# Kernel tuning notes

Measured on AMD Instinct MI355X. Metric: run time of the kernel, lower is better.

## Reference

```python
import jax, jax.numpy as jnp
import numpy as np

SEED_ID = 1234  # seed_id from init, masked to 32 bits


def _synth_R(k_iter, d_out, d_in, dtype):
    # Seeded pseudo-random base weight: randn(d_out, d_in) / sqrt(d_in)
    s = (SEED_ID ^ int(k_iter)) & 0xFFFFFFFF
    R = jax.random.normal(jax.random.key(s), (d_out, d_in), dtype=dtype)
    return R * np.float32(1.0 / np.sqrt(d_in))


def setup_inputs() -> dict:
    key = jax.random.key(0)
    kx, kv, ku = jax.random.split(key, 3)
    B, S, D, RANK = 32, 4096, 512, 64
    x = jax.random.normal(kx, (B, S, D), dtype=jnp.float32)
    alpha = jnp.float32(1.0)
    U = jnp.zeros((D, RANK), dtype=jnp.float32)
    # match torch init: V ~ N(0,1)/sqrt(rank)
    V = jax.random.normal(kv, (RANK, D), dtype=jnp.float32) * np.float32(1.0 / np.sqrt(RANK))
    bias = jnp.zeros((D,), dtype=jnp.float32)
    return {"x": x, "alpha": alpha, "U": U, "V": V, "bias": bias, "k_iter": 2}


def reference(x, alpha, U, V, bias, k_iter):
    d_out = U.shape[0]
    d_in = V.shape[1]
    dtype = x.dtype
    R = _synth_R(k_iter, d_out, d_in, dtype)                      # [d_out, d_in]
    W = alpha.astype(dtype) * R + (U.astype(dtype) @ V.astype(dtype))  # [d_out, d_in]
    # F.linear: x @ W.T + b
    return jnp.einsum('bsd,od->bso', x, W) + bias.astype(dtype)
```

## Files before the change

kernel.cpp:

```cpp
#include <hip/hip_runtime.h>
#include <stdint.h>


#define M_TOTAL 131072
#define N_DIM 512
#define K_DIM 512
#define RANK 64

#define BM 128
#define BK 32
#define NKT (K_DIM / BK)

#define AOFF(p) ((p)*16384)
#define WOFF(p) (32768 + (p)*32768)

typedef __attribute__((ext_vector_type(8))) short bf16x8;
typedef __attribute__((ext_vector_type(4))) float f32x4;

__device__ __forceinline__ void threefry2x32(uint32_t k0, uint32_t k1,
                                             uint32_t x0, uint32_t x1,
                                             uint32_t& y0, uint32_t& y1) {
  uint32_t ks2 = k0 ^ k1 ^ 0x1BD11BDAu;
  const uint32_t ks[3] = {k0, k1, ks2};
  const int R0[4] = {13, 15, 26, 6};
  const int R1[4] = {17, 29, 16, 24};
  x0 += ks[0];
  x1 += ks[1];
#pragma unroll
  for (int g = 0; g < 5; ++g) {
    const int* r = (g & 1) ? R1 : R0;
#pragma unroll
    for (int i = 0; i < 4; ++i) {
      x0 += x1;
      x1 = (x1 << r[i]) | (x1 >> (32 - r[i]));
      x1 ^= x0;
    }
    x0 += ks[(g + 1) % 3];
    x1 += ks[(g + 2) % 3] + (uint32_t)(g + 1);
  }
  y0 = x0;
  y1 = x1;
}

__device__ __forceinline__ float erfinv_f32(float x) {
  float w = -log1pf(-x * x);
  float p;
  if (w < 5.0f) {
    w = w - 2.5f;
    p = 2.81022636e-08f;
    p = fmaf(p, w, 3.43273939e-07f);
    p = fmaf(p, w, -3.5233877e-06f);
    p = fmaf(p, w, -4.39150654e-06f);
    p = fmaf(p, w, 0.00021858087f);
    p = fmaf(p, w, -0.00125372503f);
    p = fmaf(p, w, -0.00417768164f);
    p = fmaf(p, w, 0.246640727f);
    p = fmaf(p, w, 1.50140941f);
  } else {
    w = sqrtf(w) - 3.0f;
    p = -0.000200214257f;
    p = fmaf(p, w, 0.000100950558f);
    p = fmaf(p, w, 0.00134934322f);
    p = fmaf(p, w, -0.00367342844f);
    p = fmaf(p, w, 0.00573950773f);
    p = fmaf(p, w, -0.0076224613f);
    p = fmaf(p, w, 0.00943887047f);
    p = fmaf(p, w, 1.00167406f);
    p = fmaf(p, w, 2.83297682f);
  }
  return p * x;
}

__device__ __forceinline__ unsigned short f32_to_bf16_rtne(float f) {
  uint32_t x = __float_as_uint(f);
  uint32_t r = (x + 0x7FFFu + ((x >> 16) & 1u)) >> 16;
  return (unsigned short)r;
}

__global__ __launch_bounds__(256) void build_w_kernel(
    const float* __restrict__ alpha_p, const float* __restrict__ U,
    const float* __restrict__ V, const int* __restrict__ k_iter_p,
    unsigned short* __restrict__ Wb) {
  int idx = blockIdx.x * blockDim.x + threadIdx.x;
  uint32_t s = (1234u ^ (uint32_t)(*k_iter_p));
  uint32_t y0, y1;
  threefry2x32(0u, s, 0u, (uint32_t)idx, y0, y1);
  uint32_t bits = y0 ^ y1;
  float u01 = __uint_as_float((bits >> 9) | 0x3f800000u) - 1.0f;
  const float lo = -0.99999994f;
  float u = fmaxf(lo, u01 * 2.0f + lo);
  float rnorm = 1.41421354f * erfinv_f32(u);
  const float scale = 0.044194173824159216f;

  int o = idx >> 9;
  int i = idx & 511;
  float uv = 0.0f;
#pragma unroll 8
  for (int r = 0; r < RANK; ++r)
    uv = fmaf(U[o * RANK + r], V[r * N_DIM + i], uv);

  float w = (*alpha_p) * (rnorm * scale) + uv;
  Wb[idx] = f32_to_bf16_rtne(w);
}

__device__ __forceinline__ void gload16(const void* g, void* l) {
  __builtin_amdgcn_global_load_lds(
      (const __attribute__((address_space(1))) void*)g,
      (__attribute__((address_space(3))) void*)l, 16, 0, 0);
}

__device__ __forceinline__ bf16x8 cvt8(const float4& lo, const float4& hi) {
  union {
    bf16x8 v;
    uint32_t d[4];
  } au;
  asm("v_cvt_pk_bf16_f32 %0, %1, %2" : "=v"(au.d[0]) : "v"(lo.x), "v"(lo.y));
  asm("v_cvt_pk_bf16_f32 %0, %1, %2" : "=v"(au.d[1]) : "v"(lo.z), "v"(lo.w));
  asm("v_cvt_pk_bf16_f32 %0, %1, %2" : "=v"(au.d[2]) : "v"(hi.x), "v"(hi.y));
  asm("v_cvt_pk_bf16_f32 %0, %1, %2" : "=v"(au.d[3]) : "v"(hi.z), "v"(hi.w));
  return au.v;
}

__global__ __launch_bounds__(512, 2) void gemm_kernel(
    const float* __restrict__ X, const unsigned short* __restrict__ Wb,
    const float* __restrict__ bias, float* __restrict__ Out) {
  extern __shared__ char smem[];

  const int tid = threadIdx.x;
  const int lane = tid & 63;
  const int wave = tid >> 6;
  const int wm = wave >> 2;
  const int wn = wave & 3;
  const size_t m0 = (size_t)blockIdx.x * BM;

  const char* pA[2];
#pragma unroll
  for (int c = 0; c < 2; ++c) {
    int slot = c * 512 + tid;
    int row = slot >> 3, q = slot & 7;
    int gcol = (q ^ ((row & 3) << 1)) * 4;
    pA[c] = (const char*)(X + (m0 + row) * K_DIM + gcol);
  }
  const char* pW[4];
#pragma unroll
  for (int c = 0; c < 4; ++c) {
    int slot = c * 512 + tid;
    int row = slot >> 2, q = slot & 3;
    int gcol = (q ^ (row & 3)) * 8;
    pW[c] = (const char*)(Wb + (size_t)row * K_DIM + gcol);
  }
  const int ldsA_base = wave * 1024;
  const int ldsW_base = wave * 1024;

#define STAGE(p_)                                                        \
  {                                                                      \
    _Pragma("unroll") for (int c = 0; c < 2; ++c)                        \
        gload16(pA[c], smem + AOFF(p_) + c * 8192 + ldsA_base);          \
    _Pragma("unroll") for (int c = 0; c < 4; ++c)                        \
        gload16(pW[c], smem + WOFF(p_) + c * 8192 + ldsW_base);          \
  }
#define ADVANCE()                                                        \
  {                                                                      \
    _Pragma("unroll") for (int c = 0; c < 2; ++c) pA[c] += 128;          \
    _Pragma("unroll") for (int c = 0; c < 4; ++c) pW[c] += 64;           \
  }

  const int r = lane & 15;
  const int g = lane >> 4;
  int offA[4];
#pragma unroll
  for (int i = 0; i < 4; ++i) {
    int row = wm * 64 + i * 16 + r;
    offA[i] = row * 128 + ((2 * g) ^ ((r & 3) << 1)) * 16;
  }
  int offW[8];
#pragma unroll
  for (int j = 0; j < 8; ++j) {
    int row = wn * 128 + j * 16 + r;
    offW[j] = row * 64 + (g ^ (r & 3)) * 16;
  }

  f32x4 acc[4][8];
#pragma unroll
  for (int i = 0; i < 4; ++i)
#pragma unroll
    for (int j = 0; j < 8; ++j) acc[i][j] = (f32x4){0.f, 0.f, 0.f, 0.f};

  STAGE(0)
  __syncthreads();

#pragma unroll
  for (int kt = 0; kt < NKT; ++kt) {
    if (kt < NKT - 1) {
      ADVANCE()
      STAGE((kt + 1) & 1)
    }

    bf16x8 xa[4];
#pragma unroll
    for (int i = 0; i < 4; ++i) {
      const char* a = smem + AOFF(kt & 1) + offA[i];
      float4 lo = *reinterpret_cast<const float4*>(a);
      float4 hi = *reinterpret_cast<const float4*>(a + 16);
      xa[i] = cvt8(lo, hi);
    }
#pragma unroll
    for (int j = 0; j < 8; ++j) {
      bf16x8 wb = *reinterpret_cast<const bf16x8*>(smem + WOFF(kt & 1) + offW[j]);
#pragma unroll
      for (int i = 0; i < 4; ++i)
        acc[i][j] = __builtin_amdgcn_mfma_f32_16x16x32_bf16(wb, xa[i],
                                                            acc[i][j], 0, 0, 0);
    }

    if (kt < NKT - 1)
      __syncthreads();
  }

#pragma unroll
  for (int i = 0; i < 4; ++i) {
    const size_t rowoff = (m0 + wm * 64 + i * 16 + r) * N_DIM;
#pragma unroll
    for (int j = 0; j < 8; ++j) {
      const int c0 = wn * 128 + j * 16 + g * 4;
      float4 bv = *reinterpret_cast<const float4*>(&bias[c0]);
      float4 o;
      o.x = acc[i][j][0] + bv.x;
      o.y = acc[i][j][1] + bv.y;
      o.z = acc[i][j][2] + bv.z;
      o.w = acc[i][j][3] + bv.w;
      *reinterpret_cast<float4*>(&Out[rowoff + c0]) = o;
    }
  }
#undef STAGE
#undef ADVANCE
}

extern "C" void kernel_launch(void* const* d_in, const int* in_sizes, int n_in,
                              void* d_out, int out_size, void* d_ws,
                              size_t ws_size, hipStream_t stream) {
  (void)in_sizes;
  (void)n_in;
  (void)out_size;
  (void)ws_size;
  const float* x = (const float*)d_in[0];
  const float* alpha = (const float*)d_in[1];
  const float* U = (const float*)d_in[2];
  const float* V = (const float*)d_in[3];
  const float* bias = (const float*)d_in[4];
  const int* k_iter = (const int*)d_in[5];
  float* out = (float*)d_out;
  unsigned short* Wb = (unsigned short*)d_ws;

  build_w_kernel<<<(N_DIM * K_DIM) / 256, 256, 0, stream>>>(alpha, U, V,
                                                            k_iter, Wb);

  const int lds_bytes = 98304;
  hipFuncSetAttribute((const void*)gemm_kernel,
                      hipFuncAttributeMaxDynamicSharedMemorySize, lds_bytes);
  const int grid = M_TOTAL / BM;
  gemm_kernel<<<grid, 512, lds_bytes, stream>>>(x, Wb, bias, out);
}
```

Baseline: 167.1 us.

## Triple-buffer GEMM LDS staging with two-deep prefetch and vmcnt waits

The GEMM moves from double to triple buffering of the A and W tiles in LDS. It prefetches two k-tiles ahead. Each iteration waits on vmcnt so only the oldest stage must have landed, then uses a single raw s_barrier instead of two __syncthreads. The aim is to hide more global-load latency on the memory-bound streaming of x. The cost is raising dynamic LDS to 144 KB per block and relying on hand-counted vmcnt values that must match the six loads issued per stage.

```diff
diff --git a/kernel.cpp b/kernel.cpp
--- a/kernel.cpp
+++ b/kernel.cpp
@@ -11,8 +11,8 @@
 #define BK 32
 #define NKT (K_DIM / BK)
 
-#define AOFF(p) ((p)*16384)
-#define WOFF(p) (32768 + (p)*32768)
+#define AOFF(b) ((b)*16384)
+#define WOFF(b) (49152 + (b)*32768)
 
 typedef __attribute__((ext_vector_type(8))) short bf16x8;
 typedef __attribute__((ext_vector_type(4))) float f32x4;
@@ -152,17 +152,12 @@
   const int ldsA_base = wave * 1024;
   const int ldsW_base = wave * 1024;
 
-#define STAGE(p_)                                                        \
-  {                                                                      \
-    _Pragma("unroll") for (int c = 0; c < 2; ++c)                        \
-        gload16(pA[c], smem + AOFF(p_) + c * 8192 + ldsA_base);          \
-    _Pragma("unroll") for (int c = 0; c < 4; ++c)                        \
-        gload16(pW[c], smem + WOFF(p_) + c * 8192 + ldsW_base);          \
-  }
-#define ADVANCE()                                                        \
-  {                                                                      \
-    _Pragma("unroll") for (int c = 0; c < 2; ++c) pA[c] += 128;          \
-    _Pragma("unroll") for (int c = 0; c < 4; ++c) pW[c] += 64;           \
+#define STAGE(buf_, kt_)                                                     \
+  {                                                                          \
+    _Pragma("unroll") for (int c = 0; c < 2; ++c)                            \
+        gload16(pA[c] + (kt_)*128, smem + AOFF(buf_) + c * 8192 + ldsA_base);\
+    _Pragma("unroll") for (int c = 0; c < 4; ++c)                            \
+        gload16(pW[c] + (kt_)*64, smem + WOFF(buf_) + c * 8192 + ldsW_base); \
   }
 
   const int r = lane & 15;
@@ -186,35 +181,38 @@
 #pragma unroll
     for (int j = 0; j < 8; ++j) acc[i][j] = (f32x4){0.f, 0.f, 0.f, 0.f};
 
-  STAGE(0)
-  __syncthreads();
+  STAGE(0, 0)
+  STAGE(1, 1)
 
 #pragma unroll
   for (int kt = 0; kt < NKT; ++kt) {
-    if (kt < NKT - 1) {
-      ADVANCE()
-      STAGE((kt + 1) & 1)
-    }
-
+    if (kt < NKT - 1)
+      asm volatile("s_waitcnt vmcnt(6)" ::: "memory");
+    else
+      asm volatile("s_waitcnt vmcnt(0)" ::: "memory");
+    __builtin_amdgcn_sched_barrier(0);
+    __builtin_amdgcn_s_barrier();
+    __builtin_amdgcn_sched_barrier(0);
+
+    if (kt < NKT - 2) STAGE((kt + 2) % 3, kt + 2)
+
+    const int b = kt % 3;
     bf16x8 xa[4];
 #pragma unroll
     for (int i = 0; i < 4; ++i) {
-      const char* a = smem + AOFF(kt & 1) + offA[i];
+      const char* a = smem + AOFF(b) + offA[i];
       float4 lo = *reinterpret_cast<const float4*>(a);
       float4 hi = *reinterpret_cast<const float4*>(a + 16);
       xa[i] = cvt8(lo, hi);
     }
 #pragma unroll
     for (int j = 0; j < 8; ++j) {
-      bf16x8 wb = *reinterpret_cast<const bf16x8*>(smem + WOFF(kt & 1) + offW[j]);
+      bf16x8 wb = *reinterpret_cast<const bf16x8*>(smem + WOFF(b) + offW[j]);
 #pragma unroll
       for (int i = 0; i < 4; ++i)
         acc[i][j] = __builtin_amdgcn_mfma_f32_16x16x32_bf16(wb, xa[i],
                                                             acc[i][j], 0, 0, 0);
     }
-
-    if (kt < NKT - 1)
-      __syncthreads();
   }
 
 #pragma unroll
@@ -233,7 +231,6 @@
     }
   }
 #undef STAGE
-#undef ADVANCE
 }
 
 extern "C" void kernel_launch(void* const* d_in, const int* in_sizes, int n_in,
@@ -255,7 +252,7 @@
   build_w_kernel<<<(N_DIM * K_DIM) / 256, 256, 0, stream>>>(alpha, U, V,
                                                             k_iter, Wb);
 
-  const int lds_bytes = 98304;
+  const int lds_bytes = 147456;
   hipFuncSetAttribute((const void*)gemm_kernel,
                       hipFuncAttributeMaxDynamicSharedMemorySize, lds_bytes);
   const int grid = M_TOTAL / BM;
```

Result: slower. 181.0 us (+8.3%).
